# Kernel tuning notes

Measured on AMD Instinct MI355X. Metric: run time of the kernel, lower is better.

The kernel has to match this reference:

```python
import jax, jax.numpy as jnp
import numpy as np

N = 200000
W = 255  # hidden width hard-coded in the module


def _linear_params(key, fan_in, fan_out, w_std=0.02, b_val=0.0):
    kw, _ = jax.random.split(key)
    w = jax.random.normal(kw, (fan_in, fan_out), dtype=jnp.float32) * w_std
    b = jnp.full((fan_out,), b_val, dtype=jnp.float32)
    return w, b


def setup_inputs() -> dict:
    key = jax.random.key(0)
    ks = jax.random.split(key, 20)
    inp = {
        "opacity_emb": jax.random.normal(ks[0], (N, 1), dtype=jnp.float32),
        "shs_emb": jax.random.normal(ks[1], (N, 16, 3), dtype=jnp.float32),
        "time_emb": jax.random.uniform(ks[2], (N, 1), dtype=jnp.float32),
        "semantic_feature": jax.random.normal(ks[3], (N, 128), dtype=jnp.float32),
        "point": jax.random.normal(ks[4], (N, 3), dtype=jnp.float32),
        "scales_input": jax.random.normal(ks[5], (N, 3), dtype=jnp.float32),
        "rotations_input": jax.random.normal(ks[6], (N, 4), dtype=jnp.float32),
        "dx": jax.random.normal(ks[7], (N, 3), dtype=jnp.float32),
    }
    # mask_net: ReLU -> Linear(W,W) -> ReLU -> Linear(W,1) -> sigmoid
    inp["mask_w1"], inp["mask_b1"] = _linear_params(ks[8], W, W)
    inp["mask_w2"], inp["mask_b2"] = _linear_params(ks[9], W, 1)
    # deform heads: ReLU -> Linear(W,W) -> ReLU -> Linear(W,out)
    inp["pos_w1"], inp["pos_b1"] = _linear_params(ks[10], W, W)
    inp["pos_w2"], inp["pos_b2"] = _linear_params(ks[11], W, 3)
    inp["scl_w1"], inp["scl_b1"] = _linear_params(ks[12], W, W)
    inp["scl_w2"], inp["scl_b2"] = _linear_params(ks[13], W, 3)
    inp["rot_w1"], inp["rot_b1"] = _linear_params(ks[14], W, W)
    inp["rot_w2"], inp["rot_b2"] = _linear_params(ks[15], W, 4)
    inp["shs_w1"], inp["shs_b1"] = _linear_params(ks[16], W, W)
    inp["shs_w2"], inp["shs_b2"] = _linear_params(ks[17], W, 48)
    return inp


def _head(hidden, w1, b1, w2, b2):
    # ReLU -> Linear -> ReLU -> Linear (matches nn.Sequential in the module)
    h = jax.nn.relu(hidden)
    h = jax.nn.relu(h @ w1 + b1)
    return h @ w2 + b2


def _time_pos_enc(time_emb, n):
    # vectorized version of the scalar sin/cos for-loop: uses only time_emb[0, 0]
    t = time_emb[0, 0]
    i = jnp.arange(0, 64, 2, dtype=jnp.float32)          # even indices
    freq = jnp.power(jnp.float32(10000.0), i / jnp.float32(32.0))  # 10000**(2*i/64)
    enc = jnp.stack([jnp.sin(t / freq), jnp.cos(t / freq)], axis=1).reshape(64)
    return jnp.broadcast_to(enc[None, :], (n, 64))


def reference(opacity_emb, shs_emb, time_emb, semantic_feature, point,
              scales_input, rotations_input, dx,
              mask_w1, mask_b1, mask_w2, mask_b2,
              pos_w1, pos_b1, pos_w2, pos_b2,
              scl_w1, scl_b1, scl_w2, scl_b2,
              rot_w1, rot_b1, rot_w2, rot_b2,
              shs_w1, shs_b1, shs_w2, shs_b2):
    n = shs_emb.shape[0]
    shs_flat = shs_emb.reshape(n, 48)
    tpe = _time_pos_enc(time_emb, n)                     # [N, 64]
    hidden = jnp.concatenate(
        (point, rotations_input, scales_input, opacity_emb,
         shs_flat, semantic_feature, dx, time_emb, tpe), axis=1)  # [N, 255]

    mask = jax.nn.sigmoid(_head(hidden, mask_w1, mask_b1, mask_w2, mask_b2))  # [N, 1]

    dx_out = _head(hidden, pos_w1, pos_b1, pos_w2, pos_b2)        # [N, 3]
    pts = point + dx_out * mask

    ds = _head(hidden, scl_w1, scl_b1, scl_w2, scl_b2)            # [N, 3]
    scales = scales_input + ds * mask

    dr = _head(hidden, rot_w1, rot_b1, rot_w2, rot_b2)            # [N, 4]
    rotations = rotations_input + dr * mask

    opacity = opacity_emb[:, :1]

    dshs = _head(hidden, shs_w1, shs_b1, shs_w2, shs_b2).reshape(n, 16, 3)
    shs = shs_emb + dshs * mask[:, :, None]

    return (pts, scales, rotations, opacity, shs, dx_out, dshs)
```

## Files before the change

kernel.cpp:

```cpp
#include <hip/hip_runtime.h>
#include <math.h>

typedef unsigned short u16;
typedef __attribute__((ext_vector_type(8))) short short8;
typedef __attribute__((ext_vector_type(4))) float floatx4;

__device__ __forceinline__ u16 f2bf(float f) {
    union { float f; unsigned u; } v; v.f = f;
    unsigned r = v.u + 0x7fffu + ((v.u >> 16) & 1u);
    return (u16)(r >> 16);
}

struct WPtrs {
    const float* w1[5];
    const float* w2[5];
};

typedef const __attribute__((address_space(1))) unsigned GUA;
typedef __attribute__((address_space(3))) unsigned LUA;

__device__ __forceinline__ void stage_w1(const u16* gbase, u16* lbase, int wave, int lane) {
    const char* g = (const char*)gbase;
    char* l = (char*)lbase;
#pragma unroll
    for (int i = 0; i < 16; ++i) {
        int off = (wave * 16 + i) * 1024;
        __builtin_amdgcn_global_load_lds((GUA*)(g + off + lane * 16), (LUA*)(l + off), 16, 0, 0);
    }
}

__global__ void prep_weights(WPtrs p, const float* __restrict__ te,
                             u16* __restrict__ W1t, u16* __restrict__ W2t,
                             u16* __restrict__ enc)
{
    const int bid = blockIdx.x;
    const int tid = threadIdx.x;
    if (bid < 80) {
        __shared__ float tile[64 * 65];
        int h = bid / 16, t = bid % 16;
        int k0 = (t / 4) * 64, n0 = (t % 4) * 64;
        int nn = tid & 63, g = tid >> 6;
        const float* w1 = p.w1[h];
#pragma unroll
        for (int rep = 0; rep < 16; ++rep) {
            int kl = g * 16 + rep;
            int k = k0 + kl, nidx = n0 + nn;
            float v = (k < 255 && nidx < 255) ? w1[k * 255 + nidx] : 0.0f;
            tile[kl * 65 + nn] = v;
        }
        __syncthreads();
#pragma unroll
        for (int i = 0; i < 2; ++i) {
            int c = tid * 2 + i;
            int nl = c >> 3, kcl = c & 7;
            int n = n0 + nl;
            int kcg = (k0 >> 3) + kcl;
            short8 sv;
#pragma unroll
            for (int j = 0; j < 8; ++j)
                sv[j] = (short)f2bf(tile[(kcl * 8 + j) * 65 + nl]);
            *(short8*)(W1t + h * 65536 + n * 256 + (((kcg ^ (n & 31))) << 3)) = sv;
        }
    } else if (bid < 192) {
        int row = bid - 80;
        int h, roff, od;
        if (row < 16)      { h = 0; roff = 0;  od = 1; }
        else if (row < 32) { h = 1; roff = 16; od = 3; }
        else if (row < 48) { h = 2; roff = 32; od = 3; }
        else if (row < 64) { h = 3; roff = 48; od = 4; }
        else               { h = 4; roff = 64; od = 48; }
        int n2 = row - roff;
        int k = tid;
        float v = (k < 255 && n2 < od) ? p.w2[h][k * od + n2] : 0.0f;
        W2t[row * 256 + k] = f2bf(v);
    } else {
        if (tid < 64) {
            float t = te[0];
            float fi = (float)(tid & ~1);
            float freq = powf(10000.0f, fi * (1.0f / 32.0f));
            float a = t / freq;
            float v = (tid & 1) ? cosf(a) : sinf(a);
            enc[tid] = f2bf(fmaxf(v, 0.0f));
        }
    }
}

struct FusedArgs {
    const u16* W1t; const u16* W2t; const u16* enc;
    const float* b1[5]; const float* b2[5];
    const float* opa; const float* shs; const float* te; const float* sem;
    const float* pt;  const float* scl; const float* rot; const float* dxp;
    float* out; int n;
};

__device__ __forceinline__ short8 gather8(const FusedArgs& A, int row, int c0)
{
    short8 sv;
    if (c0 >= 64 && c0 <= 176) {
        const float* s = A.sem + (size_t)row * 128 + (c0 - 59);
        float4 a = *(const float4*)(s);
        float4 b = *(const float4*)(s + 4);
        sv[0] = (short)f2bf(fmaxf(a.x, 0.f)); sv[1] = (short)f2bf(fmaxf(a.y, 0.f));
        sv[2] = (short)f2bf(fmaxf(a.z, 0.f)); sv[3] = (short)f2bf(fmaxf(a.w, 0.f));
        sv[4] = (short)f2bf(fmaxf(b.x, 0.f)); sv[5] = (short)f2bf(fmaxf(b.y, 0.f));
        sv[6] = (short)f2bf(fmaxf(b.z, 0.f)); sv[7] = (short)f2bf(fmaxf(b.w, 0.f));
    } else if (c0 >= 192) {
#pragma unroll
        for (int j = 0; j < 8; ++j) {
            int c = c0 + j;
            sv[j] = (c < 255) ? (short)A.enc[c - 191] : (short)0;
        }
    } else {
#pragma unroll
        for (int j = 0; j < 8; ++j) {
            int c = c0 + j;
            float v;
            if (c < 3)        v = A.pt[row * 3 + c];
            else if (c < 7)   v = A.rot[row * 4 + (c - 3)];
            else if (c < 10)  v = A.scl[row * 3 + (c - 7)];
            else if (c < 11)  v = A.opa[row];
            else if (c < 59)  v = A.shs[(size_t)row * 48 + (c - 11)];
            else if (c < 187) v = A.sem[(size_t)row * 128 + (c - 59)];
            else if (c < 190) v = A.dxp[row * 3 + (c - 187)];
            else if (c < 191) v = A.te[row];
            else { sv[j] = (short)A.enc[c - 191]; continue; }
            sv[j] = (short)f2bf(fmaxf(v, 0.0f));
        }
    }
    return sv;
}

__device__ __forceinline__ void layer1_part(const short8 (&xf)[2][8], const u16* W1L,
                                            int part, int q, int ln, floatx4 (&acc)[8][2])
{
#pragma unroll
    for (int ct = 0; ct < 8; ++ct) {
        acc[ct][0] = (floatx4){0.f, 0.f, 0.f, 0.f};
        acc[ct][1] = (floatx4){0.f, 0.f, 0.f, 0.f};
    }
#pragma unroll
    for (int kk = 0; kk < 8; ++kk) {
#pragma unroll
        for (int ct = 0; ct < 8; ++ct) {
            int nidx = part * 128 + ct * 16 + ln;
            int sw = (kk * 4 + q) ^ (nidx & 31);
            short8 wf = *(const short8*)(W1L + nidx * 256 + (sw << 3));
            acc[ct][0] = __builtin_amdgcn_mfma_f32_16x16x32_bf16(wf, xf[0][kk], acc[ct][0], 0, 0, 0);
            acc[ct][1] = __builtin_amdgcn_mfma_f32_16x16x32_bf16(wf, xf[1][kk], acc[ct][1], 0, 0, 0);
        }
    }
}

template<int MT>
__device__ __forceinline__ void layer2_part(floatx4 (&acc)[8][2], const float* __restrict__ b1h,
                                            const u16* __restrict__ w2th, int part, int q, int ln,
                                            floatx4 (&acc2)[3][2])
{
#pragma unroll
    for (int ct = 0; ct < 8; ++ct) {
        floatx4 b4;
        if (part == 1 && ct == 7) {
            if (q == 3) {
                b4.x = b1h[252]; b4.y = b1h[253]; b4.z = b1h[254]; b4.w = 0.f;
            } else {
                b4 = *(const floatx4*)(b1h + 240 + q * 4);
            }
        } else {
            b4 = *(const floatx4*)(b1h + part * 128 + ct * 16 + q * 4);
        }
#pragma unroll
        for (int t = 0; t < 2; ++t) {
            floatx4 v = acc[ct][t];
            v.x = fmaxf(v.x + b4.x, 0.f);
            v.y = fmaxf(v.y + b4.y, 0.f);
            v.z = fmaxf(v.z + b4.z, 0.f);
            v.w = fmaxf(v.w + b4.w, 0.f);
            acc[ct][t] = v;
        }
    }
    if (part == 0) {
#pragma unroll
        for (int mt = 0; mt < MT; ++mt) {
            acc2[mt][0] = (floatx4){0.f, 0.f, 0.f, 0.f};
            acc2[mt][1] = (floatx4){0.f, 0.f, 0.f, 0.f};
        }
    }
#pragma unroll
    for (int ks = 0; ks < 4; ++ks) {
        int ksg = part * 4 + ks;
        short8 a2[MT];
#pragma unroll
        for (int mt = 0; mt < MT; ++mt)
            a2[mt] = *(const short8*)(w2th + (mt * 16 + ln) * 256 + ksg * 32 + q * 8);
#pragma unroll
        for (int t = 0; t < 2; ++t) {
            short8 bfrag;
#pragma unroll
            for (int j = 0; j < 8; ++j) {
                int idx = (((q * 2 + (j >> 2)) & 3) << 4) | ln;
                float v0 = __shfl(acc[ks * 2 + 0][t][j & 3], idx, 64);
                float v1 = __shfl(acc[ks * 2 + 1][t][j & 3], idx, 64);
                float v = (q >> 1) ? v1 : v0;
                bfrag[j] = (short)f2bf(v);
            }
#pragma unroll
            for (int mt = 0; mt < MT; ++mt)
                acc2[mt][t] = __builtin_amdgcn_mfma_f32_16x16x32_bf16(a2[mt], bfrag, acc2[mt][t], 0, 0, 0);
        }
    }
}

__global__ __launch_bounds__(512, 2) void fused_all(FusedArgs A)
{
    extern __shared__ char smem[];
    u16* W1L = (u16*)smem;

    const int tid = threadIdx.x;
    const int wave = tid >> 6;
    const int lane = tid & 63;
    const int q = lane >> 4, ln = lane & 15;
    const int n = A.n;
    const size_t NN = (size_t)n;

    stage_w1(A.W1t, W1L, wave, lane);

    const int r0 = blockIdx.x * 256 + wave * 32;
    const int ra  = min(r0 + ln, n - 1);
    const int rbb = min(r0 + 16 + ln, n - 1);

    short8 xf[2][8];
#pragma unroll
    for (int kk = 0; kk < 8; ++kk) {
        int c0 = kk * 32 + q * 8;
        xf[0][kk] = gather8(A, ra, c0);
        xf[1][kk] = gather8(A, rbb, c0);
    }

    floatx4 acc[8][2];
    floatx4 acc2[3][2];
    float mk0 = 0.f, mk1 = 0.f, mkb0 = 0.f, mkb1 = 0.f;

    __syncthreads();

#pragma unroll 1
    for (int h = 0; h < 5; ++h) {
        const float* b1h = A.b1[h];
        const u16* w2th = A.W2t + ((h < 4) ? h * 16 : 64) * 256;

        layer1_part(xf, W1L, 0, q, ln, acc);
        if (h == 4) layer2_part<3>(acc, b1h, w2th, 0, q, ln, acc2);
        else        layer2_part<1>(acc, b1h, w2th, 0, q, ln, acc2);
        layer1_part(xf, W1L, 1, q, ln, acc);

        __syncthreads();
        if (h < 4) stage_w1(A.W1t + (h + 1) * 65536, W1L, wave, lane);

        if (h == 4) layer2_part<3>(acc, b1h, w2th, 1, q, ln, acc2);
        else        layer2_part<1>(acc, b1h, w2th, 1, q, ln, acc2);

        if (h == 0) {
            if (q == 0) {
                float bb = A.b2[0][0];
                int g0 = r0 + ln, g1 = r0 + 16 + ln;
                if (g0 < n) {
                    mk0 = 1.0f / (1.0f + expf(-(acc2[0][0][0] + bb)));
                    A.out[10 * NN + g0] = A.opa[g0];
                }
                if (g1 < n) {
                    mk1 = 1.0f / (1.0f + expf(-(acc2[0][1][0] + bb)));
                    A.out[10 * NN + g1] = A.opa[g1];
                }
            }
            mkb0 = __shfl(mk0, ln, 64);
            mkb1 = __shfl(mk1, ln, 64);
        } else if (h < 4) {
            if (q == 0) {
                const float* b2h = A.b2[h];
#pragma unroll
                for (int t = 0; t < 2; ++t) {
                    int grow = r0 + 16 * t + ln;
                    float mk = t ? mkb1 : mkb0;
                    if (grow < n) {
                        if (h == 1) {
#pragma unroll
                            for (int r = 0; r < 3; ++r) {
                                float raw = acc2[0][t][r] + b2h[r];
                                A.out[59 * NN + (size_t)grow * 3 + r] = raw;
                                A.out[(size_t)grow * 3 + r] = A.pt[(size_t)grow * 3 + r] + raw * mk;
                            }
                        } else if (h == 2) {
#pragma unroll
                            for (int r = 0; r < 3; ++r) {
                                float raw = acc2[0][t][r] + b2h[r];
                                A.out[3 * NN + (size_t)grow * 3 + r] = A.scl[(size_t)grow * 3 + r] + raw * mk;
                            }
                        } else {
#pragma unroll
                            for (int r = 0; r < 4; ++r) {
                                float raw = acc2[0][t][r] + b2h[r];
                                A.out[6 * NN + (size_t)grow * 4 + r] = A.rot[(size_t)grow * 4 + r] + raw * mk;
                            }
                        }
                    }
                }
            }
        } else {
            const float* b2h = A.b2[4];
#pragma unroll
            for (int t = 0; t < 2; ++t) {
                int grow = r0 + 16 * t + ln;
                float mk = t ? mkb1 : mkb0;
                if (grow < n) {
#pragma unroll
                    for (int mt = 0; mt < 3; ++mt) {
                        int n2b = mt * 16 + q * 4;
                        floatx4 b2v = *(const floatx4*)(b2h + n2b);
                        floatx4 raw = acc2[mt][t] + b2v;
                        *(floatx4*)(A.out + 62 * NN + (size_t)grow * 48 + n2b) = raw;
                        floatx4 s = *(const floatx4*)(A.shs + (size_t)grow * 48 + n2b);
                        *(floatx4*)(A.out + 11 * NN + (size_t)grow * 48 + n2b) = s + raw * mk;
                    }
                }
            }
        }

        if (h < 4) __syncthreads();
    }
}

extern "C" void kernel_launch(void* const* d_in, const int* in_sizes, int n_in,
                              void* d_out, int out_size, void* d_ws, size_t ws_size,
                              hipStream_t stream)
{
    const float* opa  = (const float*)d_in[0];
    const float* shs  = (const float*)d_in[1];
    const float* te   = (const float*)d_in[2];
    const float* sem  = (const float*)d_in[3];
    const float* pt   = (const float*)d_in[4];
    const float* scl  = (const float*)d_in[5];
    const float* rot  = (const float*)d_in[6];
    const float* dx   = (const float*)d_in[7];

    WPtrs p;
    p.w1[0] = (const float*)d_in[8];  p.w2[0] = (const float*)d_in[10];
    p.w1[1] = (const float*)d_in[12]; p.w2[1] = (const float*)d_in[14];
    p.w1[2] = (const float*)d_in[16]; p.w2[2] = (const float*)d_in[18];
    p.w1[3] = (const float*)d_in[20]; p.w2[3] = (const float*)d_in[22];
    p.w1[4] = (const float*)d_in[24]; p.w2[4] = (const float*)d_in[26];

    const int n = in_sizes[0];

    char* ws = (char*)d_ws;
    u16* W1t = (u16*)ws;
    u16* W2t = W1t + 5 * 65536;
    u16* enc = W2t + 112 * 256;

    prep_weights<<<193, 256, 0, stream>>>(p, te, W1t, W2t, enc);

    FusedArgs A;
    A.W1t = W1t; A.W2t = W2t; A.enc = enc;
    A.b1[0] = (const float*)d_in[9];  A.b2[0] = (const float*)d_in[11];
    A.b1[1] = (const float*)d_in[13]; A.b2[1] = (const float*)d_in[15];
    A.b1[2] = (const float*)d_in[17]; A.b2[2] = (const float*)d_in[19];
    A.b1[3] = (const float*)d_in[21]; A.b2[3] = (const float*)d_in[23];
    A.b1[4] = (const float*)d_in[25]; A.b2[4] = (const float*)d_in[27];
    A.opa = opa; A.shs = shs; A.te = te; A.sem = sem;
    A.pt = pt; A.scl = scl; A.rot = rot; A.dxp = dx;
    A.out = (float*)d_out; A.n = n;

    int grid = (n + 255) / 256;
    fused_all<<<grid, 512, 131072, stream>>>(A);
}
```

Baseline: 627.3 us.

## Stream W1 in double-buffered 32KB chunks, shrink rows per block, fp32 small heads

The kernel no longer stages a full 128KB W1 head in LDS. It streams each head's weight matrix in four 64-column chunks through two 32KB LDS buffers, prefetching the next chunk while the current one runs. Each wave now handles 16 rows instead of 32, blocks cover 128 rows, and launch bounds allow 4 blocks per CU. The small output heads (mask, pos, scale, rot) are computed with fp32 FMAs against a new fp32 copy of W2 plus cross-lane reductions instead of MFMA. This should raise occupancy and overlap weight loading with compute, but it costs a block barrier per chunk and twice as many weight reads per row processed.

```diff
diff --git a/kernel.cpp b/kernel.cpp
--- a/kernel.cpp
+++ b/kernel.cpp
@@ -19,19 +19,19 @@
 typedef const __attribute__((address_space(1))) unsigned GUA;
 typedef __attribute__((address_space(3))) unsigned LUA;
 
-__device__ __forceinline__ void stage_w1(const u16* gbase, u16* lbase, int wave, int lane) {
+__device__ __forceinline__ void stage32(const u16* gbase, u16* lbase, int wave, int lane) {
     const char* g = (const char*)gbase;
     char* l = (char*)lbase;
 #pragma unroll
-    for (int i = 0; i < 16; ++i) {
-        int off = (wave * 16 + i) * 1024;
+    for (int i = 0; i < 4; ++i) {
+        int off = (wave * 4 + i) * 1024;
         __builtin_amdgcn_global_load_lds((GUA*)(g + off + lane * 16), (LUA*)(l + off), 16, 0, 0);
     }
 }
 
 __global__ void prep_weights(WPtrs p, const float* __restrict__ te,
                              u16* __restrict__ W1t, u16* __restrict__ W2t,
-                             u16* __restrict__ enc)
+                             float* __restrict__ W2f, u16* __restrict__ enc)
 {
     const int bid = blockIdx.x;
     const int tid = threadIdx.x;
@@ -73,6 +73,10 @@
         int k = tid;
         float v = (k < 255 && n2 < od) ? p.w2[h][k * od + n2] : 0.0f;
         W2t[row * 256 + k] = f2bf(v);
+        if (h < 4 && n2 < od) {
+            int r11b = (h == 0) ? 0 : (h == 1) ? 1 : (h == 2) ? 4 : 7;
+            W2f[(r11b + n2) * 256 + k] = v;
+        }
     } else {
         if (tid < 64) {
             float t = te[0];
@@ -86,7 +90,7 @@
 }
 
 struct FusedArgs {
-    const u16* W1t; const u16* W2t; const u16* enc;
+    const u16* W1t; const u16* W2t; const float* W2f; const u16* enc;
     const float* b1[5]; const float* b2[5];
     const float* opa; const float* shs; const float* te; const float* sem;
     const float* pt;  const float* scl; const float* rot; const float* dxp;
@@ -130,90 +134,9 @@
     return sv;
 }
 
-__device__ __forceinline__ void layer1_part(const short8 (&xf)[2][8], const u16* W1L,
-                                            int part, int q, int ln, floatx4 (&acc)[8][2])
+__global__ __launch_bounds__(512, 4) void fused_all(FusedArgs A)
 {
-#pragma unroll
-    for (int ct = 0; ct < 8; ++ct) {
-        acc[ct][0] = (floatx4){0.f, 0.f, 0.f, 0.f};
-        acc[ct][1] = (floatx4){0.f, 0.f, 0.f, 0.f};
-    }
-#pragma unroll
-    for (int kk = 0; kk < 8; ++kk) {
-#pragma unroll
-        for (int ct = 0; ct < 8; ++ct) {
-            int nidx = part * 128 + ct * 16 + ln;
-            int sw = (kk * 4 + q) ^ (nidx & 31);
-            short8 wf = *(const short8*)(W1L + nidx * 256 + (sw << 3));
-            acc[ct][0] = __builtin_amdgcn_mfma_f32_16x16x32_bf16(wf, xf[0][kk], acc[ct][0], 0, 0, 0);
-            acc[ct][1] = __builtin_amdgcn_mfma_f32_16x16x32_bf16(wf, xf[1][kk], acc[ct][1], 0, 0, 0);
-        }
-    }
-}
-
-template<int MT>
-__device__ __forceinline__ void layer2_part(floatx4 (&acc)[8][2], const float* __restrict__ b1h,
-                                            const u16* __restrict__ w2th, int part, int q, int ln,
-                                            floatx4 (&acc2)[3][2])
-{
-#pragma unroll
-    for (int ct = 0; ct < 8; ++ct) {
-        floatx4 b4;
-        if (part == 1 && ct == 7) {
-            if (q == 3) {
-                b4.x = b1h[252]; b4.y = b1h[253]; b4.z = b1h[254]; b4.w = 0.f;
-            } else {
-                b4 = *(const floatx4*)(b1h + 240 + q * 4);
-            }
-        } else {
-            b4 = *(const floatx4*)(b1h + part * 128 + ct * 16 + q * 4);
-        }
-#pragma unroll
-        for (int t = 0; t < 2; ++t) {
-            floatx4 v = acc[ct][t];
-            v.x = fmaxf(v.x + b4.x, 0.f);
-            v.y = fmaxf(v.y + b4.y, 0.f);
-            v.z = fmaxf(v.z + b4.z, 0.f);
-            v.w = fmaxf(v.w + b4.w, 0.f);
-            acc[ct][t] = v;
-        }
-    }
-    if (part == 0) {
-#pragma unroll
-        for (int mt = 0; mt < MT; ++mt) {
-            acc2[mt][0] = (floatx4){0.f, 0.f, 0.f, 0.f};
-            acc2[mt][1] = (floatx4){0.f, 0.f, 0.f, 0.f};
-        }
-    }
-#pragma unroll
-    for (int ks = 0; ks < 4; ++ks) {
-        int ksg = part * 4 + ks;
-        short8 a2[MT];
-#pragma unroll
-        for (int mt = 0; mt < MT; ++mt)
-            a2[mt] = *(const short8*)(w2th + (mt * 16 + ln) * 256 + ksg * 32 + q * 8);
-#pragma unroll
-        for (int t = 0; t < 2; ++t) {
-            short8 bfrag;
-#pragma unroll
-            for (int j = 0; j < 8; ++j) {
-                int idx = (((q * 2 + (j >> 2)) & 3) << 4) | ln;
-                float v0 = __shfl(acc[ks * 2 + 0][t][j & 3], idx, 64);
-                float v1 = __shfl(acc[ks * 2 + 1][t][j & 3], idx, 64);
-                float v = (q >> 1) ? v1 : v0;
-                bfrag[j] = (short)f2bf(v);
-            }
-#pragma unroll
-            for (int mt = 0; mt < MT; ++mt)
-                acc2[mt][t] = __builtin_amdgcn_mfma_f32_16x16x32_bf16(a2[mt], bfrag, acc2[mt][t], 0, 0, 0);
-        }
-    }
-}
-
-__global__ __launch_bounds__(512, 2) void fused_all(FusedArgs A)
-{
-    extern __shared__ char smem[];
-    u16* W1L = (u16*)smem;
+    __shared__ u16 W1L[2][16384];
 
     const int tid = threadIdx.x;
     const int wave = tid >> 6;
@@ -222,109 +145,159 @@
     const int n = A.n;
     const size_t NN = (size_t)n;
 
-    stage_w1(A.W1t, W1L, wave, lane);
-
-    const int r0 = blockIdx.x * 256 + wave * 32;
-    const int ra  = min(r0 + ln, n - 1);
-    const int rbb = min(r0 + 16 + ln, n - 1);
-
-    short8 xf[2][8];
-#pragma unroll
-    for (int kk = 0; kk < 8; ++kk) {
-        int c0 = kk * 32 + q * 8;
-        xf[0][kk] = gather8(A, ra, c0);
-        xf[1][kk] = gather8(A, rbb, c0);
-    }
-
-    floatx4 acc[8][2];
-    floatx4 acc2[3][2];
-    float mk0 = 0.f, mk1 = 0.f, mkb0 = 0.f, mkb1 = 0.f;
+    stage32(A.W1t, W1L[0], wave, lane);
+
+    const int r0 = blockIdx.x * 128 + wave * 16;
+    const int ra = min(r0 + ln, n - 1);
+    const int grow = r0 + ln;
+
+    short8 xf[8];
+#pragma unroll
+    for (int kk = 0; kk < 8; ++kk)
+        xf[kk] = gather8(A, ra, kk * 32 + q * 8);
 
     __syncthreads();
 
+    floatx4 acc[4];
+    floatx4 acc2[3];
+    float out2[4];
+    float mkb = 0.f;
+
 #pragma unroll 1
-    for (int h = 0; h < 5; ++h) {
+    for (int c = 0; c < 20; ++c) {
+        const int h = c >> 2;
+        const int Q = c & 3;
+        if (c + 1 < 20)
+            stage32(A.W1t + (size_t)(c + 1) * 16384, W1L[(c + 1) & 1], wave, lane);
+        const u16* buf = W1L[c & 1];
+
+#pragma unroll
+        for (int ct = 0; ct < 4; ++ct) acc[ct] = (floatx4){0.f, 0.f, 0.f, 0.f};
+#pragma unroll
+        for (int kk = 0; kk < 8; ++kk) {
+#pragma unroll
+            for (int ct = 0; ct < 4; ++ct) {
+                int nl = ct * 16 + ln;
+                int sw = (kk * 4 + q) ^ (nl & 31);
+                short8 wf = *(const short8*)(buf + nl * 256 + (sw << 3));
+                acc[ct] = __builtin_amdgcn_mfma_f32_16x16x32_bf16(wf, xf[kk], acc[ct], 0, 0, 0);
+            }
+        }
+
         const float* b1h = A.b1[h];
-        const u16* w2th = A.W2t + ((h < 4) ? h * 16 : 64) * 256;
-
-        layer1_part(xf, W1L, 0, q, ln, acc);
-        if (h == 4) layer2_part<3>(acc, b1h, w2th, 0, q, ln, acc2);
-        else        layer2_part<1>(acc, b1h, w2th, 0, q, ln, acc2);
-        layer1_part(xf, W1L, 1, q, ln, acc);
-
-        __syncthreads();
-        if (h < 4) stage_w1(A.W1t + (h + 1) * 65536, W1L, wave, lane);
-
-        if (h == 4) layer2_part<3>(acc, b1h, w2th, 1, q, ln, acc2);
-        else        layer2_part<1>(acc, b1h, w2th, 1, q, ln, acc2);
-
-        if (h == 0) {
-            if (q == 0) {
-                float bb = A.b2[0][0];
-                int g0 = r0 + ln, g1 = r0 + 16 + ln;
-                if (g0 < n) {
-                    mk0 = 1.0f / (1.0f + expf(-(acc2[0][0][0] + bb)));
-                    A.out[10 * NN + g0] = A.opa[g0];
-                }
-                if (g1 < n) {
-                    mk1 = 1.0f / (1.0f + expf(-(acc2[0][1][0] + bb)));
-                    A.out[10 * NN + g1] = A.opa[g1];
-                }
-            }
-            mkb0 = __shfl(mk0, ln, 64);
-            mkb1 = __shfl(mk1, ln, 64);
-        } else if (h < 4) {
-            if (q == 0) {
+#pragma unroll
+        for (int ct = 0; ct < 4; ++ct) {
+            floatx4 b4;
+            if (Q == 3 && ct == 3) {
+                if (q == 3) { b4.x = b1h[252]; b4.y = b1h[253]; b4.z = b1h[254]; b4.w = 0.f; }
+                else        b4 = *(const floatx4*)(b1h + 240 + q * 4);
+            } else {
+                b4 = *(const floatx4*)(b1h + Q * 64 + ct * 16 + q * 4);
+            }
+            floatx4 v = acc[ct];
+            v.x = fmaxf(v.x + b4.x, 0.f);
+            v.y = fmaxf(v.y + b4.y, 0.f);
+            v.z = fmaxf(v.z + b4.z, 0.f);
+            v.w = fmaxf(v.w + b4.w, 0.f);
+            acc[ct] = v;
+        }
+
+        if (h < 4) {
+            const int od = (h == 0) ? 1 : (h == 3) ? 4 : 3;
+            const int r11b = (h == 0) ? 0 : (h == 1) ? 1 : (h == 2) ? 4 : 7;
+            if (Q == 0) {
+#pragma unroll
+                for (int m = 0; m < 4; ++m) out2[m] = 0.f;
+            }
+            const float* wb = A.W2f + r11b * 256 + Q * 64 + q * 4;
+#pragma unroll
+            for (int n2 = 0; n2 < 4; ++n2) {
+                if (n2 < od) {
+#pragma unroll
+                    for (int ct = 0; ct < 4; ++ct) {
+                        floatx4 w4 = *(const floatx4*)(wb + n2 * 256 + ct * 16);
+                        out2[n2] = fmaf(acc[ct].x, w4.x, out2[n2]);
+                        out2[n2] = fmaf(acc[ct].y, w4.y, out2[n2]);
+                        out2[n2] = fmaf(acc[ct].z, w4.z, out2[n2]);
+                        out2[n2] = fmaf(acc[ct].w, w4.w, out2[n2]);
+                    }
+                }
+            }
+            if (Q == 3) {
+#pragma unroll
+                for (int n2 = 0; n2 < 4; ++n2) {
+                    float v = out2[n2];
+                    v += __shfl_xor(v, 16, 64);
+                    v += __shfl_xor(v, 32, 64);
+                    out2[n2] = v;
+                }
                 const float* b2h = A.b2[h];
-#pragma unroll
-                for (int t = 0; t < 2; ++t) {
-                    int grow = r0 + 16 * t + ln;
-                    float mk = t ? mkb1 : mkb0;
-                    if (grow < n) {
-                        if (h == 1) {
-#pragma unroll
-                            for (int r = 0; r < 3; ++r) {
-                                float raw = acc2[0][t][r] + b2h[r];
-                                A.out[59 * NN + (size_t)grow * 3 + r] = raw;
-                                A.out[(size_t)grow * 3 + r] = A.pt[(size_t)grow * 3 + r] + raw * mk;
-                            }
-                        } else if (h == 2) {
-#pragma unroll
-                            for (int r = 0; r < 3; ++r) {
-                                float raw = acc2[0][t][r] + b2h[r];
-                                A.out[3 * NN + (size_t)grow * 3 + r] = A.scl[(size_t)grow * 3 + r] + raw * mk;
-                            }
-                        } else {
-#pragma unroll
-                            for (int r = 0; r < 4; ++r) {
-                                float raw = acc2[0][t][r] + b2h[r];
-                                A.out[6 * NN + (size_t)grow * 4 + r] = A.rot[(size_t)grow * 4 + r] + raw * mk;
-                            }
+                if (h == 0) {
+                    mkb = 1.0f / (1.0f + expf(-(out2[0] + b2h[0])));
+                    if (q == 0 && grow < n) A.out[10 * NN + grow] = A.opa[grow];
+                } else if (grow < n && q == 0) {
+                    if (h == 1) {
+#pragma unroll
+                        for (int r = 0; r < 3; ++r) {
+                            float raw = out2[r] + b2h[r];
+                            A.out[59 * NN + (size_t)grow * 3 + r] = raw;
+                            A.out[(size_t)grow * 3 + r] = A.pt[(size_t)grow * 3 + r] + raw * mkb;
+                        }
+                    } else if (h == 2) {
+#pragma unroll
+                        for (int r = 0; r < 3; ++r) {
+                            float raw = out2[r] + b2h[r];
+                            A.out[3 * NN + (size_t)grow * 3 + r] = A.scl[(size_t)grow * 3 + r] + raw * mkb;
+                        }
+                    } else {
+#pragma unroll
+                        for (int r = 0; r < 4; ++r) {
+                            float raw = out2[r] + b2h[r];
+                            A.out[6 * NN + (size_t)grow * 4 + r] = A.rot[(size_t)grow * 4 + r] + raw * mkb;
                         }
                     }
                 }
             }
         } else {
-            const float* b2h = A.b2[4];
-#pragma unroll
-            for (int t = 0; t < 2; ++t) {
-                int grow = r0 + 16 * t + ln;
-                float mk = t ? mkb1 : mkb0;
-                if (grow < n) {
-#pragma unroll
-                    for (int mt = 0; mt < 3; ++mt) {
-                        int n2b = mt * 16 + q * 4;
-                        floatx4 b2v = *(const floatx4*)(b2h + n2b);
-                        floatx4 raw = acc2[mt][t] + b2v;
-                        *(floatx4*)(A.out + 62 * NN + (size_t)grow * 48 + n2b) = raw;
-                        floatx4 s = *(const floatx4*)(A.shs + (size_t)grow * 48 + n2b);
-                        *(floatx4*)(A.out + 11 * NN + (size_t)grow * 48 + n2b) = s + raw * mk;
-                    }
-                }
-            }
-        }
-
-        if (h < 4) __syncthreads();
+            if (Q == 0) {
+#pragma unroll
+                for (int mt = 0; mt < 3; ++mt) acc2[mt] = (floatx4){0.f, 0.f, 0.f, 0.f};
+            }
+            const u16* w2th = A.W2t + 64 * 256;
+#pragma unroll
+            for (int ks = 0; ks < 2; ++ks) {
+                int ksg = Q * 2 + ks;
+                short8 a2[3];
+#pragma unroll
+                for (int mt = 0; mt < 3; ++mt)
+                    a2[mt] = *(const short8*)(w2th + (mt * 16 + ln) * 256 + ksg * 32 + q * 8);
+                short8 bfrag;
+#pragma unroll
+                for (int j = 0; j < 8; ++j) {
+                    int idx = (((q * 2 + (j >> 2)) & 3) << 4) | ln;
+                    float v0 = __shfl(acc[ks * 2 + 0][j & 3], idx, 64);
+                    float v1 = __shfl(acc[ks * 2 + 1][j & 3], idx, 64);
+                    bfrag[j] = (short)f2bf((q >> 1) ? v1 : v0);
+                }
+#pragma unroll
+                for (int mt = 0; mt < 3; ++mt)
+                    acc2[mt] = __builtin_amdgcn_mfma_f32_16x16x32_bf16(a2[mt], bfrag, acc2[mt], 0, 0, 0);
+            }
+            if (Q == 3 && grow < n) {
+                const float* b2h = A.b2[4];
+#pragma unroll
+                for (int mt = 0; mt < 3; ++mt) {
+                    int n2b = mt * 16 + q * 4;
+                    floatx4 b2v = *(const floatx4*)(b2h + n2b);
+                    floatx4 raw = acc2[mt] + b2v;
+                    *(floatx4*)(A.out + 62 * NN + (size_t)grow * 48 + n2b) = raw;
+                    floatx4 s = *(const floatx4*)(A.shs + (size_t)grow * 48 + n2b);
+                    *(floatx4*)(A.out + 11 * NN + (size_t)grow * 48 + n2b) = s + raw * mkb;
+                }
+            }
+        }
+
+        __syncthreads();
     }
 }
 
@@ -351,14 +324,15 @@
     const int n = in_sizes[0];
 
     char* ws = (char*)d_ws;
-    u16* W1t = (u16*)ws;
-    u16* W2t = W1t + 5 * 65536;
-    u16* enc = W2t + 112 * 256;
-
-    prep_weights<<<193, 256, 0, stream>>>(p, te, W1t, W2t, enc);
+    u16*   W1t = (u16*)ws;
+    u16*   W2t = W1t + 5 * 65536;
+    float* W2f = (float*)(ws + 655360 + 57344);
+    u16*   enc = (u16*)(ws + 655360 + 57344 + 11264);
+
+    prep_weights<<<193, 256, 0, stream>>>(p, te, W1t, W2t, W2f, enc);
 
     FusedArgs A;
-    A.W1t = W1t; A.W2t = W2t; A.enc = enc;
+    A.W1t = W1t; A.W2t = W2t; A.W2f = W2f; A.enc = enc;
     A.b1[0] = (const float*)d_in[9];  A.b2[0] = (const float*)d_in[11];
     A.b1[1] = (const float*)d_in[13]; A.b2[1] = (const float*)d_in[15];
     A.b1[2] = (const float*)d_in[17]; A.b2[2] = (const float*)d_in[19];
@@ -368,6 +342,6 @@
     A.pt = pt; A.scl = scl; A.rot = rot; A.dxp = dx;
     A.out = (float*)d_out; A.n = n;
 
-    int grid = (n + 255) / 256;
-    fused_all<<<grid, 512, 131072, stream>>>(A);
-}
+    int grid = (n + 127) / 128;
+    fused_all<<<grid, 512, 0, stream>>>(A);
+}
```

Result: faster. 600.2 us (-4.3%).
